# Kernel tuning notes

Hardware: AMD Instinct MI355X
Metric: run time of the kernel (lower is better)

## Reference

```python
import jax, jax.numpy as jnp
import numpy as np

B, T, D, E, K = 2, 2048, 1024, 8, 2
H = 2 * D  # expert hidden

def setup_inputs() -> dict:
    key = jax.random.key(0)
    ks = jax.random.split(key, 5)
    s = 0.02
    return {
        "x": jax.random.normal(ks[0], (B, T, D), jnp.float32),
        "Wr": jax.random.normal(ks[1], (D, E), jnp.float32) * s,
        "br": jnp.zeros((E,), jnp.float32),
        "W1": jax.random.normal(ks[2], (E, D, H), jnp.float32) * s,
        "b1": jnp.zeros((E, H), jnp.float32),
        "W2": jax.random.normal(ks[3], (E, H, D), jnp.float32) * s,
        "b2": jnp.zeros((E, D), jnp.float32),
    }

def reference(x, Wr, br, W1, b1, W2, b2):
    # Router: logits -> top-k -> sparse softmax gates (non-top-k get 0 weight)
    logits = jnp.einsum('btd,de->bte', x, Wr) + br            # [B,T,E]
    topv, topi = jax.lax.top_k(logits, K)                      # [B,T,K]
    sel_mask = (jax.nn.one_hot(topi, E, dtype=logits.dtype).sum(-2) > 0)  # [B,T,E]
    neg_inf = jnp.finfo(logits.dtype).min
    gates = jax.nn.softmax(jnp.where(sel_mask, logits, neg_inf), axis=-1)  # [B,T,E], zero off top-k
    # Experts: final = sum_e gate[...,e] * Expert_e(x). Gate is exactly 0 for
    # non-selected experts, so dense-per-expert compute gives identical math to
    # the gather/scatter loop in the torch module. Dropout is identity (eval).
    h = jax.nn.relu(jnp.einsum('btd,edh->bteh', x, W1) + b1)   # [B,T,E,H]
    out = jnp.einsum('bte,bteh,ehd->btd', gates, h, W2)
    out = out + jnp.einsum('bte,ed->btd', gates, b2)
    return out
```

## Files before the change

### kernel.cpp

```cpp
#include <hip/hip_runtime.h>
#include <hip/hip_bf16.h>
#include <math.h>

namespace {

constexpr int NTOK   = 4096;
constexpr int DDIM   = 1024;
constexpr int E      = 8;
constexpr int HDIM   = 2048;
constexpr int MAXROWS = 8192;
constexpr int MAXBLK  = 56;

typedef __bf16 bf16;
typedef __attribute__((ext_vector_type(8))) __bf16 bf16x8;
typedef __attribute__((ext_vector_type(4))) float floatx4;
typedef __attribute__((ext_vector_type(4))) int   i32x4;

__device__ inline void gload_lds16(const bf16* g, bf16* l) {
  __builtin_amdgcn_global_load_lds(
      (const __attribute__((address_space(1))) void*)g,
      (__attribute__((address_space(3))) void*)l, 16, 0, 0);
}

__device__ inline bf16x8 ds_read16(const bf16* p) {
  i32x4 r;
  asm volatile("ds_read_b128 %0, %1"
               : "=v"(r)
               : "v"((const __attribute__((address_space(3))) bf16*)p));
  return __builtin_bit_cast(bf16x8, r);
}

__device__ inline unsigned short bfbits(float f) {
  return __builtin_bit_cast(unsigned short, (bf16)f);
}

__device__ inline void transpose_tile128(const float* __restrict__ src,
                                         bf16* __restrict__ dst,
                                         int R, int C, int c0, int r0,
                                         unsigned short (*tileT)[136]) {
  int tid = threadIdx.x;
  int rp = (tid >> 4) * 2;
  int tc = (tid & 15) * 4;
  float4 v0[4], v1[4];
#pragma unroll
  for (int i = 0; i < 4; ++i) {
    int r = rp + i * 32;
    v0[i] = *(const float4*)(src + (size_t)(r0 + r)     * C + c0 + tc);
    v1[i] = *(const float4*)(src + (size_t)(r0 + r + 1) * C + c0 + tc);
  }
#pragma unroll
  for (int i = 0; i < 4; ++i) {
    int r = rp + i * 32;
#pragma unroll
    for (int q = 0; q < 4; ++q) {
      int c = tc + q;
      int xorv = ((c >> 2) & 7) << 3;
      float a = ((const float*)&v0[i])[q];
      float b = ((const float*)&v1[i])[q];
      *(unsigned int*)&tileT[c][r ^ xorv] =
          (unsigned int)bfbits(a) | ((unsigned int)bfbits(b) << 16);
    }
  }
  __syncthreads();
  int tc2 = (tid & 15) * 8;
  int tr2 = tid >> 4;
#pragma unroll
  for (int i = 0; i < 4; ++i) {
    int c = tr2 + i * 16;
    int xorv = ((c >> 2) & 7) << 3;
    *(bf16x8*)(dst + (size_t)(c0 + c) * R + r0 + tc2) =
        *(const bf16x8*)&tileT[c][tc2 ^ xorv];
  }
}

__global__ __launch_bounds__(256) void prep_kernel(
    const float* __restrict__ x,  const float* __restrict__ Wr,
    const float* __restrict__ br, const float* __restrict__ W1,
    const float* __restrict__ W2,
    int* __restrict__ topk_e, float* __restrict__ topk_g,
    bf16* __restrict__ xb, bf16* __restrict__ W1T, bf16* __restrict__ W2T) {
  __shared__ unsigned short tileT[64][136];
  int b = blockIdx.x;
  if (b < 2048) {
    int bx = b & 31, by = (b >> 5) & 7, bz = b >> 8;
    const float* src = W1 + (size_t)bz * DDIM * HDIM;
    bf16* dst = W1T + (size_t)bz * DDIM * HDIM;
    transpose_tile128(src, dst, DDIM, HDIM, bx * 64, by * 128, tileT);
    return;
  }
  if (b < 4096) {
    int lb = b - 2048;
    int bx = lb & 15, by = (lb >> 4) & 15, bz = lb >> 8;
    const float* src = W2 + (size_t)bz * DDIM * HDIM;
    bf16* dst = W2T + (size_t)bz * DDIM * HDIM;
    transpose_tile128(src, dst, HDIM, DDIM, bx * 64, by * 128, tileT);
    return;
  }
  int rb = b - 4096;
  int wave = threadIdx.x >> 6;
  int lane = threadIdx.x & 63;
  int t0 = (rb * 4 + wave) * 2;

  float acc[16];
#pragma unroll
  for (int j = 0; j < 16; ++j) acc[j] = 0.f;

#pragma unroll
  for (int i = 0; i < DDIM / 64; ++i) {
    int d = i * 64 + lane;
    float4 w0 = *(const float4*)(Wr + (size_t)d * E);
    float4 w1 = *(const float4*)(Wr + (size_t)d * E + 4);
#pragma unroll
    for (int t = 0; t < 2; ++t) {
      float xv = x[(size_t)(t0 + t) * DDIM + d];
      xb[(size_t)(t0 + t) * DDIM + d] = (bf16)xv;
      acc[t * 8 + 0] += xv * w0.x; acc[t * 8 + 1] += xv * w0.y;
      acc[t * 8 + 2] += xv * w0.z; acc[t * 8 + 3] += xv * w0.w;
      acc[t * 8 + 4] += xv * w1.x; acc[t * 8 + 5] += xv * w1.y;
      acc[t * 8 + 6] += xv * w1.z; acc[t * 8 + 7] += xv * w1.w;
    }
  }
#pragma unroll
  for (int off = 32; off > 0; off >>= 1) {
#pragma unroll
    for (int j = 0; j < 16; ++j) acc[j] += __shfl_xor(acc[j], off, 64);
  }
  if (lane == 0) {
#pragma unroll
    for (int t = 0; t < 2; ++t) {
      int tt = t0 + t;
      float lg[E];
#pragma unroll
      for (int e = 0; e < E; ++e) lg[e] = acc[t * 8 + e] + br[e];
      int e0 = 0;
#pragma unroll
      for (int e = 1; e < E; ++e) if (lg[e] > lg[e0]) e0 = e;
      int e1 = (e0 == 0) ? 1 : 0;
#pragma unroll
      for (int e = 0; e < E; ++e) if (e != e0 && lg[e] > lg[e1]) e1 = e;
      float ex = expf(lg[e1] - lg[e0]);
      float s = 1.f + ex;
      topk_e[2 * tt]     = e0;
      topk_e[2 * tt + 1] = e1;
      topk_g[2 * tt]     = 1.f / s;
      topk_g[2 * tt + 1] = ex / s;
    }
  }
}

__global__ __launch_bounds__(1024) void scan_scatter_kernel(
    const int* __restrict__ topk_e,
    int* __restrict__ counts,
    int* __restrict__ offsets,
    int* __restrict__ blockmap,
    int* __restrict__ rowtok, int* __restrict__ tokrow) {
  __shared__ int hist[E], curs[E];
  int tid = threadIdx.x;
  int lane = tid & 63;
  unsigned long long lt = ((unsigned long long)1 << lane) - 1;
  if (tid < E) hist[tid] = 0;
  __syncthreads();
  for (int i = tid; i < 2 * NTOK; i += 1024) {
    int e = topk_e[i];
#pragma unroll
    for (int ee = 0; ee < E; ++ee) {
      unsigned long long m = __ballot(e == ee);
      if (m && lane == __ffsll((long long)m) - 1) atomicAdd(&hist[ee], __popcll(m));
    }
  }
  __syncthreads();
  int h[E], pre[E + 1], nt[E], tb[E + 1];
  pre[0] = 0; tb[0] = 0;
#pragma unroll
  for (int e = 0; e < E; ++e) {
    h[e] = hist[e];
    pre[e + 1] = pre[e] + h[e];
    nt[e] = (h[e] + 191) / 192;
    tb[e + 1] = tb[e] + nt[e];
  }
  int nb = tb[E];
  if (tid < E) { counts[tid * 16] = h[tid]; curs[tid] = pre[tid]; }
  if (tid < E + 1) offsets[tid] = pre[tid];
  if (tid < MAXBLK) {
    int xc = tid / 7, j = tid % 7;
    int lo = (nb * xc) >> 3, hi = (nb * (xc + 1)) >> 3;
    int idx = lo + j, v = -1;
    if (idx < hi) {
      int e = 0;
#pragma unroll
      for (int k = 1; k < E; ++k) if (idx >= tb[k]) e = k;
      v = (e << 16) | (idx - tb[e]);
    }
    blockmap[tid] = v;
  }
  __syncthreads();
  for (int i = tid; i < 2 * NTOK; i += 1024) {
    int e = topk_e[i];
#pragma unroll
    for (int ee = 0; ee < E; ++ee) {
      unsigned long long m = __ballot(e == ee);
      if (m) {
        int leader = __ffsll((long long)m) - 1;
        int base = 0;
        if (lane == leader) base = atomicAdd(&curs[ee], __popcll(m));
        base = __shfl(base, leader, 64);
        if (e == ee) {
          int row = base + __popcll(m & lt);
          rowtok[row] = i >> 1;
          tokrow[i] = row;
        }
      }
    }
  }
}

template <bool GATHER, bool RELU>
__global__ __launch_bounds__(256, 2) void ffn_gemm(
    const bf16* __restrict__ A, const bf16* __restrict__ W,
    const float* __restrict__ bias, bf16* __restrict__ Y,
    const int* __restrict__ rowtok, const int* __restrict__ offsets,
    const int* __restrict__ counts,
    const int* __restrict__ blockmap,
    int Kdim, int Ndim) {
  static_assert(MAXBLK == 56, "XCD chunking assumes gridDim.x == 56 == 8*7");
  int xcd = blockIdx.x & 7;
  int mq  = blockIdx.x >> 3;
  int bm = blockmap[xcd * 7 + mq];
  if (bm < 0) return;
  int e = bm >> 16;
  int mBase = (bm & 0xffff) * 192;
  int cnt = counts[e * 16];
  int rowBase = offsets[e] + mBase;
  int nBase = blockIdx.y * 128;
  int validRows = cnt - mBase; if (validRows > 192) validRows = 192;

  __shared__ bf16 Asm[2][192 * 64];
  __shared__ bf16 Bsm[2][128 * 64];

  int tid = threadIdx.x;
  int wave = tid >> 6, lane = tid & 63;
  int lrow = lane >> 3;
  int lseg = lane & 7;
  int sseg = lseg ^ lrow;

  const bf16* aptr[6];
  const bf16* bptr[4];
#pragma unroll
  for (int i = 0; i < 6; ++i) {
    int c = wave + i * 4;
    int r = rowBase + c * 8 + lrow;
    if (r > MAXROWS - 1) r = MAXROWS - 1;
    size_t rowoff = GATHER ? (size_t)rowtok[r] * Kdim : (size_t)r * Kdim;
    aptr[i] = A + rowoff + sseg * 8;
  }
#pragma unroll
  for (int i = 0; i < 4; ++i) {
    int c = wave + i * 4;
    bptr[i] = W + ((size_t)e * Ndim + nBase + c * 8 + lrow) * (size_t)Kdim + sseg * 8;
  }

  floatx4 acc[6][4];
#pragma unroll
  for (int m = 0; m < 6; ++m)
#pragma unroll
    for (int n = 0; n < 4; ++n) acc[m][n] = floatx4{0.f, 0.f, 0.f, 0.f};

  int wm = wave & 1, wn = wave >> 1;
  int mrow = lane & 15;
  int kseg0 = lane >> 4;
  int swz = mrow & 7;

  auto issue = [&](int p, int kc) {
#pragma unroll
    for (int i = 0; i < 6; ++i) {
      int c = wave + i * 4;
      gload_lds16(aptr[i] + kc, &Asm[p][c * 512]);
    }
#pragma unroll
    for (int i = 0; i < 4; ++i) {
      int c = wave + i * 4;
      gload_lds16(bptr[i] + kc, &Bsm[p][c * 512]);
    }
  };

  issue(0, 0);
  int p = 0;
  for (int kc = 0; kc < Kdim; kc += 64) {
    if (kc + 64 < Kdim) {
      issue(p ^ 1, kc + 64);
      asm volatile("s_waitcnt vmcnt(10)" ::: "memory");
    } else {
      asm volatile("s_waitcnt vmcnt(0)" ::: "memory");
    }
    asm volatile("s_barrier" ::: "memory");

#pragma unroll
    for (int ks = 0; ks < 2; ++ks) {
      int kk = (((ks << 2) | kseg0) ^ swz) << 3;
      bf16x8 af[6], bfr[4];
#pragma unroll
      for (int m = 0; m < 6; ++m)
        af[m] = ds_read16(&Asm[p][(wm * 96 + m * 16 + mrow) * 64 + kk]);
#pragma unroll
      for (int n = 0; n < 4; ++n)
        bfr[n] = ds_read16(&Bsm[p][(wn * 64 + n * 16 + mrow) * 64 + kk]);
      asm volatile("s_waitcnt lgkmcnt(0)" ::: "memory");
      __builtin_amdgcn_sched_barrier(0);
      __builtin_amdgcn_s_setprio(1);
#pragma unroll
      for (int m = 0; m < 6; ++m)
#pragma unroll
        for (int n = 0; n < 4; ++n)
          acc[m][n] = __builtin_amdgcn_mfma_f32_16x16x32_bf16(af[m], bfr[n], acc[m][n], 0, 0, 0);
      __builtin_amdgcn_s_setprio(0);
    }

    asm volatile("s_barrier" ::: "memory");
    p ^= 1;
  }

  int crow = (lane >> 4) * 4;
  int ccol = lane & 15;
#pragma unroll
  for (int n = 0; n < 4; ++n) {
    int colg = nBase + wn * 64 + n * 16 + ccol;
    float bv = bias[(size_t)e * Ndim + colg];
#pragma unroll
    for (int m = 0; m < 6; ++m) {
#pragma unroll
      for (int r = 0; r < 4; ++r) {
        int rl = wm * 96 + m * 16 + crow + r;
        if (rl < validRows) {
          float v = acc[m][n][r] + bv;
          if (RELU) v = fmaxf(v, 0.f);
          Y[(size_t)(rowBase + rl) * Ndim + colg] = (bf16)v;
        }
      }
    }
  }
}

__global__ void combine_kernel(const bf16* __restrict__ Y2,
                               const int* __restrict__ tokrow,
                               const float* __restrict__ topk_g,
                               float* __restrict__ out) {
  int idx = blockIdx.x * 256 + threadIdx.x;
  int t = idx >> 7;
  int d8 = (idx & 127) * 8;
  int r0 = tokrow[2 * t], r1 = tokrow[2 * t + 1];
  float g0 = topk_g[2 * t], g1 = topk_g[2 * t + 1];
  bf16x8 a = *(const bf16x8*)(Y2 + (size_t)r0 * DDIM + d8);
  bf16x8 b = *(const bf16x8*)(Y2 + (size_t)r1 * DDIM + d8);
  float o[8];
#pragma unroll
  for (int j = 0; j < 8; ++j) o[j] = g0 * (float)a[j] + g1 * (float)b[j];
  float* op = out + (size_t)t * DDIM + d8;
  *(float4*)op = *(float4*)&o[0];
  *(float4*)(op + 4) = *(float4*)&o[4];
}

}

extern "C" void kernel_launch(void* const* d_in, const int* in_sizes, int n_in,
                              void* d_out, int out_size, void* d_ws, size_t ws_size,
                              hipStream_t stream) {
  const float* x  = (const float*)d_in[0];
  const float* Wr = (const float*)d_in[1];
  const float* br = (const float*)d_in[2];
  const float* W1 = (const float*)d_in[3];
  const float* b1 = (const float*)d_in[4];
  const float* W2 = (const float*)d_in[5];
  const float* b2 = (const float*)d_in[6];
  float* out = (float*)d_out;

  char* w = (char*)d_ws;
  int*   counts   = (int*)(w);
  int*   offsets  = (int*)(w + 1024);
  int*   blockmap = (int*)(w + 2048);
  int*   topk_e   = (int*)(w + 4096);
  float* topk_g   = (float*)(w + 4096 + 32768);
  int*   rowtok   = (int*)(w + 4096 + 65536);
  int*   tokrow   = (int*)(w + 4096 + 98304);
  char*  big      = w + 4096 + 131072;
  bf16* xb  = (bf16*)(big);
  bf16* W1T = (bf16*)(big + 8388608);
  bf16* W2T = (bf16*)(big + 8388608 + 33554432);
  bf16* Y1  = (bf16*)(big + 8388608 + 67108864);
  bf16* Y2  = (bf16*)(big + 8388608);

  prep_kernel<<<4608, 256, 0, stream>>>(x, Wr, br, W1, W2, topk_e, topk_g, xb, W1T, W2T);
  scan_scatter_kernel<<<1, 1024, 0, stream>>>(topk_e, counts, offsets, blockmap,
                                              rowtok, tokrow);
  ffn_gemm<true, true><<<dim3(MAXBLK, HDIM / 128), 256, 0, stream>>>(
      xb, W1T, b1, Y1, rowtok, offsets, counts, blockmap, DDIM, HDIM);
  ffn_gemm<false, false><<<dim3(MAXBLK, DDIM / 128), 256, 0, stream>>>(
      Y1, W2T, b2, Y2, rowtok, offsets, counts, blockmap, HDIM, DDIM);
  combine_kernel<<<NTOK * DDIM / 8 / 256, 256, 0, stream>>>(Y2, tokrow, topk_g, out);
}
```

Before: 329.6 us.

## Move W2 transpose from prep kernel into first FFN GEMM grid

Takes the W2 fp32-to-bf16 transpose out of the prep kernel and runs it as extra blocks appended to the first expert GEMM's grid (37 extra y-rows of 56 blocks, 2048 tiles used). The transpose blocks reuse the GEMM's shared-memory buffer as their tile scratch. The aim is to overlap the memory-bound W2 conversion with the compute-bound first GEMM and to shorten the prep kernel that sits on the critical path. In exchange, the transpose blocks may compete with GEMM blocks for CU slots and bandwidth, and since higher y-indices are usually dispatched last they may end up running as a tail.

```diff
diff --git a/kernel.cpp b/kernel.cpp
--- a/kernel.cpp
+++ b/kernel.cpp
@@ -76,9 +76,8 @@
 __global__ __launch_bounds__(256) void prep_kernel(
     const float* __restrict__ x,  const float* __restrict__ Wr,
     const float* __restrict__ br, const float* __restrict__ W1,
-    const float* __restrict__ W2,
     int* __restrict__ topk_e, float* __restrict__ topk_g,
-    bf16* __restrict__ xb, bf16* __restrict__ W1T, bf16* __restrict__ W2T) {
+    bf16* __restrict__ xb, bf16* __restrict__ W1T) {
   __shared__ unsigned short tileT[64][136];
   int b = blockIdx.x;
   if (b < 2048) {
@@ -88,15 +87,7 @@
     transpose_tile128(src, dst, DDIM, HDIM, bx * 64, by * 128, tileT);
     return;
   }
-  if (b < 4096) {
-    int lb = b - 2048;
-    int bx = lb & 15, by = (lb >> 4) & 15, bz = lb >> 8;
-    const float* src = W2 + (size_t)bz * DDIM * HDIM;
-    bf16* dst = W2T + (size_t)bz * DDIM * HDIM;
-    transpose_tile128(src, dst, HDIM, DDIM, bx * 64, by * 128, tileT);
-    return;
-  }
-  int rb = b - 4096;
+  int rb = b - 2048;
   int wave = threadIdx.x >> 6;
   int lane = threadIdx.x & 63;
   int t0 = (rb * 4 + wave) * 2;
@@ -221,8 +212,25 @@
     const int* __restrict__ rowtok, const int* __restrict__ offsets,
     const int* __restrict__ counts,
     const int* __restrict__ blockmap,
+    const float* __restrict__ Tsrc, bf16* __restrict__ Tdst, int ntr,
     int Kdim, int Ndim) {
   static_assert(MAXBLK == 56, "XCD chunking assumes gridDim.x == 56 == 8*7");
+  __shared__ bf16 Asm[2][192 * 64];
+  __shared__ bf16 Bsm[2][128 * 64];
+
+  int NY = Ndim >> 7;
+  if ((int)blockIdx.y >= NY) {
+    int tb = ((int)blockIdx.y - NY) * (int)gridDim.x + (int)blockIdx.x;
+    if (tb < ntr) {
+      int bx = tb & 15, by2 = (tb >> 4) & 15, bz = tb >> 8;
+      auto tileT = (unsigned short(*)[136])(&Asm[0][0]);
+      transpose_tile128(Tsrc + (size_t)bz * DDIM * HDIM,
+                        Tdst + (size_t)bz * DDIM * HDIM,
+                        HDIM, DDIM, bx * 64, by2 * 128, tileT);
+    }
+    return;
+  }
+
   int xcd = blockIdx.x & 7;
   int mq  = blockIdx.x >> 3;
   int bm = blockmap[xcd * 7 + mq];
@@ -233,9 +241,6 @@
   int rowBase = offsets[e] + mBase;
   int nBase = blockIdx.y * 128;
   int validRows = cnt - mBase; if (validRows > 192) validRows = 192;
-
-  __shared__ bf16 Asm[2][192 * 64];
-  __shared__ bf16 Bsm[2][128 * 64];
 
   int tid = threadIdx.x;
   int wave = tid >> 6, lane = tid & 63;
@@ -388,12 +393,14 @@
   bf16* Y1  = (bf16*)(big + 8388608 + 67108864);
   bf16* Y2  = (bf16*)(big + 8388608);
 
-  prep_kernel<<<4608, 256, 0, stream>>>(x, Wr, br, W1, W2, topk_e, topk_g, xb, W1T, W2T);
+  prep_kernel<<<2560, 256, 0, stream>>>(x, Wr, br, W1, topk_e, topk_g, xb, W1T);
   scan_scatter_kernel<<<1, 1024, 0, stream>>>(topk_e, counts, offsets, blockmap,
                                               rowtok, tokrow);
-  ffn_gemm<true, true><<<dim3(MAXBLK, HDIM / 128), 256, 0, stream>>>(
-      xb, W1T, b1, Y1, rowtok, offsets, counts, blockmap, DDIM, HDIM);
+  ffn_gemm<true, true><<<dim3(MAXBLK, HDIM / 128 + 37), 256, 0, stream>>>(
+      xb, W1T, b1, Y1, rowtok, offsets, counts, blockmap,
+      W2, W2T, 2048, DDIM, HDIM);
   ffn_gemm<false, false><<<dim3(MAXBLK, DDIM / 128), 256, 0, stream>>>(
-      Y1, W2T, b2, Y2, rowtok, offsets, counts, blockmap, HDIM, DDIM);
+      Y1, W2T, b2, Y2, rowtok, offsets, counts, blockmap,
+      nullptr, nullptr, 0, HDIM, DDIM);
   combine_kernel<<<NTOK * DDIM / 8 / 256, 256, 0, stream>>>(Y2, tokrow, topk_g, out);
 }
```

New measurement: 319.9 us. 2.9% less time.
